# Kernel tuning notes

Measured on AMD Instinct MI355X. Metric: run time of the kernel, lower is better.

The kernel has to match this reference:

```python
import jax, jax.numpy as jnp
import numpy as np
from jax import lax

B, T, I, H, O = 128, 512, 256, 512, 256


def setup_inputs() -> dict:
    key = jax.random.key(0)
    ks = jax.random.split(key, 7)
    s_ih = 1.0 / np.sqrt(H)
    return {
        "inputs": jax.random.normal(ks[0], (B, T, I), dtype=jnp.float32),
        "W_ih": jax.random.uniform(ks[1], (H, I), jnp.float32, -s_ih, s_ih),
        "b_ih": jax.random.uniform(ks[2], (H,), jnp.float32, -s_ih, s_ih),
        "W_hh": jax.random.uniform(ks[3], (H, H), jnp.float32, -s_ih, s_ih),
        "b_hh": jax.random.uniform(ks[4], (H,), jnp.float32, -s_ih, s_ih),
        "W_out": jax.random.uniform(ks[5], (O, H), jnp.float32, -s_ih, s_ih),
        "b_out": jax.random.uniform(ks[6], (O,), jnp.float32, -s_ih, s_ih),
        "h0": jnp.zeros((H,), dtype=jnp.float32),
    }


def reference(inputs, W_ih, b_ih, W_hh, b_hh, W_out, b_out, h0):
    # inputs: [B, T, I]; returns readout of last hidden state: [B, O]
    Bsz, Tlen = inputs.shape[0], inputs.shape[1]
    inv_T = jnp.asarray(1.0 / Tlen, dtype=inputs.dtype)
    # Precompute input projection for all timesteps (one big GEMM):
    # x_proj[b,t,h] = inputs @ W_ih.T + b_ih + b_hh
    x_proj = jnp.einsum('bti,hi->bth', inputs, W_ih) + (b_ih + b_hh)
    x_proj_t = jnp.swapaxes(x_proj, 0, 1)  # [T, B, H]

    def step(h, xp):
        # RNNCell: tanh(xp + h @ W_hh.T); residual scaling by 1/T
        h_new = jnp.tanh(xp + h @ W_hh.T) * inv_T + h
        return h_new, None

    h_init = jnp.broadcast_to(h0, (Bsz, h0.shape[0]))
    h_last, _ = lax.scan(step, h_init, x_proj_t)
    return h_last @ W_out.T + b_out
```

## Files before the change

kernel.cpp:

```cpp
#include <hip/hip_runtime.h>
#include <stdint.h>

#define NB 128
#define NT 512
#define NI 256
#define NH 512
#define NO 256

__device__ __forceinline__ uint16_t f2bf(float x) {
  uint32_t u = __float_as_uint(x);
  return (uint16_t)((u + 0x7fffu + ((u >> 16) & 1u)) >> 16);
}
__device__ __forceinline__ uint32_t pack2bf(float a, float b) {
  return (uint32_t)f2bf(a) | ((uint32_t)f2bf(b) << 16);
}

#if __has_builtin(__builtin_amdgcn_fdot2_f32_bf16)
typedef __bf16 bf16x2_t __attribute__((ext_vector_type(2)));
#define HAVE_DOT2 1
#endif

__device__ __forceinline__ float dot2bf(uint32_t w, uint32_t h, float acc) {
#ifdef HAVE_DOT2
  return __builtin_amdgcn_fdot2_f32_bf16(__builtin_bit_cast(bf16x2_t, w),
                                         __builtin_bit_cast(bf16x2_t, h), acc, false);
#else
  float wl = __uint_as_float(w << 16), wh = __uint_as_float(w & 0xffff0000u);
  float hl = __uint_as_float(h << 16), hh = __uint_as_float(h & 0xffff0000u);
  return fmaf(wh, hh, fmaf(wl, hl, acc));
#endif
}

__device__ __forceinline__ float dot4x(uint4 w, uint4 h, float a) {
  a = dot2bf(w.x, h.x, a);
  a = dot2bf(w.y, h.y, a);
  a = dot2bf(w.z, h.z, a);
  a = dot2bf(w.w, h.w, a);
  return a;
}

__device__ __forceinline__ float fast_tanh(float x) {
  float e = __expf(2.0f * x);
#if __has_builtin(__builtin_amdgcn_rcpf)
  return 1.0f - 2.0f * __builtin_amdgcn_rcpf(e + 1.0f);
#else
  return 1.0f - 2.0f / (e + 1.0f);
#endif
}

typedef __bf16 bf16x8 __attribute__((ext_vector_type(8)));
typedef float f32x4 __attribute__((ext_vector_type(4)));

__global__ __launch_bounds__(256) void prep_kernel(const float* __restrict__ Whh,
                                                   const float* __restrict__ Wih,
                                                   const float* __restrict__ Wout,
                                                   const float* __restrict__ bih,
                                                   const float* __restrict__ bhh,
                                                   uint4* __restrict__ WQ,
                                                   float* __restrict__ WoT,
                                                   uint2* __restrict__ Wihb32,
                                                   float* __restrict__ BS) {
  int idx = blockIdx.x * 256 + threadIdx.x;
  if (idx < 32768) {
    int q = idx >> 9, t = idx & 511;
    int jj = q >> 3, c = q & 7;
    int j = (t & 63) * 8 + jj;
    int k2b = (t >> 6) * 32 + c * 4;
    const float* row = Whh + (size_t)j * NH + 2 * k2b;
    float4 f0 = *(const float4*)row;
    float4 f1 = *(const float4*)(row + 4);
    uint4 w;
    w.x = pack2bf(f0.x, f0.y);
    w.y = pack2bf(f0.z, f0.w);
    w.z = pack2bf(f1.x, f1.y);
    w.w = pack2bf(f1.z, f1.w);
    WQ[idx] = w;
  } else if (idx < 65536) {
    int i = idx - 32768;
    float4 f = *(const float4*)(Wih + (size_t)i * 4);
    uint2 p;
    p.x = pack2bf(f.x, f.y);
    p.y = pack2bf(f.z, f.w);
    Wihb32[i] = p;
  } else if (idx < 98304) {
    int i = idx - 65536;
    int o4 = (i & 63) * 4;
    int k = i >> 6;
    float4 v;
    v.x = Wout[(size_t)(o4 + 0) * NH + k];
    v.y = Wout[(size_t)(o4 + 1) * NH + k];
    v.z = Wout[(size_t)(o4 + 2) * NH + k];
    v.w = Wout[(size_t)(o4 + 3) * NH + k];
    *(float4*)&WoT[(size_t)k * NO + o4] = v;
  } else if (idx < 98816) {
    int n = idx - 98304;
    BS[n] = bih[n] + bhh[n];
  }
}

__global__ __launch_bounds__(256, 2) void xproj_kernel(const float* __restrict__ A,
                                                       const uint16_t* __restrict__ Wihb,
                                                       const float* __restrict__ BS,
                                                       uint16_t* __restrict__ XP) {
  const int w = threadIdx.x >> 6;
  const int l = threadIdx.x & 63;
  const int sl = l & 15, quad = l >> 4;
  const int m = blockIdx.x * 64 + w * 16 + sl;

  f32x4 acc[32] = {};
  const float* arow = A + (size_t)m * NI;

  for (int k0 = 0; k0 < NI; k0 += 32) {
    float4 f0 = *(const float4*)(arow + k0 + quad * 8);
    float4 f1 = *(const float4*)(arow + k0 + quad * 8 + 4);
    uint4 ap;
    ap.x = pack2bf(f0.x, f0.y);
    ap.y = pack2bf(f0.z, f0.w);
    ap.z = pack2bf(f1.x, f1.y);
    ap.w = pack2bf(f1.z, f1.w);
    bf16x8 afrag = __builtin_bit_cast(bf16x8, ap);
#pragma unroll
    for (int u = 0; u < 32; ++u) {
      uint4 bp = *(const uint4*)(Wihb + (size_t)(u * 16 + sl) * NI + k0 + quad * 8);
      acc[u] = __builtin_amdgcn_mfma_f32_16x16x32_bf16(
          __builtin_bit_cast(bf16x8, bp), afrag, acc[u], 0, 0, 0);
    }
  }

  uint16_t* xrow = XP + (size_t)m * NH;
#pragma unroll
  for (int u = 0; u < 32; ++u) {
    float4 bs = *(const float4*)(BS + u * 16 + quad * 4);
    uint2 pw;
    pw.x = pack2bf(acc[u][0] + bs.x, acc[u][1] + bs.y);
    pw.y = pack2bf(acc[u][2] + bs.z, acc[u][3] + bs.w);
    *(uint2*)(xrow + u * 16 + quad * 4) = pw;
  }
}

__global__ __launch_bounds__(512, 2) void recur_kernel(const uint4* __restrict__ WQ,
                                                       const float* __restrict__ WoT,
                                                       const uint16_t* __restrict__ XP,
                                                       const float* __restrict__ h0,
                                                       const float* __restrict__ bout,
                                                       float* __restrict__ out) {
  __shared__ uint4 WL[12][512];
  __shared__ __align__(16) uint16_t h2[2][NH];
  __shared__ float P[8][NH];
  __shared__ float hsf[NH];
  const int t = threadIdx.x;
  const int b = blockIdx.x;
  const int kq8 = t >> 6;
  const int jb = (t & 63) * 8;
  const float invT = 1.0f / (float)NT;

  uint4 Wr[52];
#pragma unroll
  for (int q = 0; q < 52; ++q) Wr[q] = WQ[q * 512 + t];
#pragma unroll
  for (int i = 0; i < 12; ++i) WL[i][t] = WQ[(52 + i) * 512 + t];

  float hj = h0[t];
  h2[0][t] = f2bf(hj);
  __syncthreads();

  const uint16_t* xpb = XP + (size_t)b * NT * NH;

  for (int ts = 0; ts < NT; ++ts) {
    const int cur = ts & 1;
    float xpj = __uint_as_float((uint32_t)xpb[(size_t)ts * NH + t] << 16);

    const uint32_t* hw = (const uint32_t*)h2[cur] + kq8 * 32;
    float a0 = 0.f, a1 = 0.f, a2 = 0.f, a3 = 0.f;
    float a4 = 0.f, a5 = 0.f, a6 = 0.f, a7 = 0.f;

    uint4 hv0 = *(const uint4*)(hw);
    uint4 hv1 = *(const uint4*)(hw + 4);
    uint4 w6n = Wr[48];
    uint4 w7n = WL[4][t];
#pragma unroll
    for (int c = 0; c < 8; ++c) {
      uint4 hv = hv0;
      hv0 = hv1;
      if (c < 6) hv1 = *(const uint4*)(hw + (c + 2) * 4);
      uint4 w6 = w6n, w7 = w7n;
      if (c < 7) {
        w6n = (c + 1 < 4) ? Wr[48 + c + 1] : WL[c - 3][t];
        w7n = WL[5 + c][t];
      }
      a0 = dot4x(Wr[c], hv, a0);
      a1 = dot4x(Wr[8 + c], hv, a1);
      a2 = dot4x(Wr[16 + c], hv, a2);
      a3 = dot4x(Wr[24 + c], hv, a3);
      a4 = dot4x(Wr[32 + c], hv, a4);
      a5 = dot4x(Wr[40 + c], hv, a5);
      a6 = dot4x(w6, hv, a6);
      a7 = dot4x(w7, hv, a7);
    }
    *(float4*)&P[kq8][jb] = make_float4(a0, a1, a2, a3);
    *(float4*)&P[kq8][jb + 4] = make_float4(a4, a5, a6, a7);
    __syncthreads();

    float y = ((P[0][t] + P[1][t]) + (P[2][t] + P[3][t])) +
              ((P[4][t] + P[5][t]) + (P[6][t] + P[7][t]));
    float hnew = fmaf(fast_tanh(xpj + y), invT, hj);
    hj = hnew;
    h2[cur ^ 1][t] = f2bf(hnew);
    __syncthreads();
  }

  hsf[t] = hj;
  __syncthreads();

  if (t < NO) {
    float c0 = 0.f, c1 = 0.f;
#pragma unroll 4
    for (int k = 0; k < NH; k += 2) {
      c0 = fmaf(WoT[(size_t)k * NO + t], hsf[k], c0);
      c1 = fmaf(WoT[(size_t)(k + 1) * NO + t], hsf[k + 1], c1);
    }
    out[(size_t)b * NO + t] = c0 + c1 + bout[t];
  }
}

extern "C" void kernel_launch(void* const* d_in, const int* in_sizes, int n_in,
                              void* d_out, int out_size, void* d_ws, size_t ws_size,
                              hipStream_t stream) {
  const float* inputs = (const float*)d_in[0];
  const float* Wih    = (const float*)d_in[1];
  const float* bih    = (const float*)d_in[2];
  const float* Whh    = (const float*)d_in[3];
  const float* bhh    = (const float*)d_in[4];
  const float* Wout   = (const float*)d_in[5];
  const float* bout   = (const float*)d_in[6];
  const float* h0     = (const float*)d_in[7];
  float* out = (float*)d_out;

  char* ws = (char*)d_ws;
  uint4*    WQ     = (uint4*)ws;
  float*    WoT    = (float*)(ws + (512u << 10));
  uint2*    Wihb32 = (uint2*)(ws + (1024u << 10));
  float*    BS     = (float*)(ws + (1280u << 10));
  uint16_t* XP     = (uint16_t*)(ws + (1536u << 10));

  hipLaunchKernelGGL(prep_kernel, dim3(386), dim3(256), 0, stream,
                     Whh, Wih, Wout, bih, bhh, WQ, WoT, Wihb32, BS);
  hipLaunchKernelGGL(xproj_kernel, dim3(NB * NT / 64), dim3(256), 0, stream,
                     inputs, (const uint16_t*)Wihb32, BS, XP);
  hipLaunchKernelGGL(recur_kernel, dim3(NB), dim3(512), 0, stream,
                     WQ, WoT, XP, h0, bout, out);
}
```

Baseline: 998.9 us.

## Process two batch rows per recurrence block to reuse register-resident W_hh

Each recurrence workgroup now advances two batch sequences at once and launches half as many blocks. Every weight fragment loaded from registers or LDS feeds two dot products, one per sequence. The aim is to halve per-step weight traffic and synchronisation per batch row, and the recurrence is latency-bound, so each block now does roughly twice the work per step. The cost is higher register pressure, since the 52 uint4 weight registers and now 16 accumulators share a launch bound of 2 blocks per CU, plus 64 blocks that may leave CUs idle.

```diff
diff --git a/kernel.cpp b/kernel.cpp
--- a/kernel.cpp
+++ b/kernel.cpp
@@ -145,11 +145,10 @@
                                                        const float* __restrict__ bout,
                                                        float* __restrict__ out) {
   __shared__ uint4 WL[12][512];
-  __shared__ __align__(16) uint16_t h2[2][NH];
-  __shared__ float P[8][NH];
-  __shared__ float hsf[NH];
+  __shared__ __align__(16) uint16_t h2[2][2][NH];
+  __shared__ float P[2][8][NH];
   const int t = threadIdx.x;
-  const int b = blockIdx.x;
+  const int b0 = blockIdx.x * 2;
   const int kq8 = t >> 6;
   const int jb = (t & 63) * 8;
   const float invT = 1.0f / (float)NT;
@@ -160,66 +159,79 @@
 #pragma unroll
   for (int i = 0; i < 12; ++i) WL[i][t] = WQ[(52 + i) * 512 + t];
 
-  float hj = h0[t];
-  h2[0][t] = f2bf(hj);
+  float hjA = h0[t];
+  float hjB = hjA;
+  {
+    uint16_t hb = f2bf(hjA);
+    h2[0][0][t] = hb;
+    h2[0][1][t] = hb;
+  }
   __syncthreads();
 
-  const uint16_t* xpb = XP + (size_t)b * NT * NH;
+  const uint16_t* xpA = XP + (size_t)b0 * NT * NH;
+  const uint16_t* xpB = XP + (size_t)(b0 + 1) * NT * NH;
 
   for (int ts = 0; ts < NT; ++ts) {
     const int cur = ts & 1;
-    float xpj = __uint_as_float((uint32_t)xpb[(size_t)ts * NH + t] << 16);
-
-    const uint32_t* hw = (const uint32_t*)h2[cur] + kq8 * 32;
-    float a0 = 0.f, a1 = 0.f, a2 = 0.f, a3 = 0.f;
-    float a4 = 0.f, a5 = 0.f, a6 = 0.f, a7 = 0.f;
-
-    uint4 hv0 = *(const uint4*)(hw);
-    uint4 hv1 = *(const uint4*)(hw + 4);
-    uint4 w6n = Wr[48];
-    uint4 w7n = WL[4][t];
+    float xA = __uint_as_float((uint32_t)xpA[(size_t)ts * NH + t] << 16);
+    float xB = __uint_as_float((uint32_t)xpB[(size_t)ts * NH + t] << 16);
+
+    const uint32_t* hwA = (const uint32_t*)h2[cur][0] + kq8 * 32;
+    const uint32_t* hwB = (const uint32_t*)h2[cur][1] + kq8 * 32;
+    float aA[8] = {}, aB[8] = {};
 #pragma unroll
     for (int c = 0; c < 8; ++c) {
-      uint4 hv = hv0;
-      hv0 = hv1;
-      if (c < 6) hv1 = *(const uint4*)(hw + (c + 2) * 4);
-      uint4 w6 = w6n, w7 = w7n;
-      if (c < 7) {
-        w6n = (c + 1 < 4) ? Wr[48 + c + 1] : WL[c - 3][t];
-        w7n = WL[5 + c][t];
+      uint4 hA = *(const uint4*)(hwA + c * 4);
+      uint4 hB = *(const uint4*)(hwB + c * 4);
+#pragma unroll
+      for (int jj = 0; jj < 6; ++jj) {
+        uint4 w = Wr[jj * 8 + c];
+        aA[jj] = dot4x(w, hA, aA[jj]);
+        aB[jj] = dot4x(w, hB, aB[jj]);
       }
-      a0 = dot4x(Wr[c], hv, a0);
-      a1 = dot4x(Wr[8 + c], hv, a1);
-      a2 = dot4x(Wr[16 + c], hv, a2);
-      a3 = dot4x(Wr[24 + c], hv, a3);
-      a4 = dot4x(Wr[32 + c], hv, a4);
-      a5 = dot4x(Wr[40 + c], hv, a5);
-      a6 = dot4x(w6, hv, a6);
-      a7 = dot4x(w7, hv, a7);
+      {
+        uint4 w = (c < 4) ? Wr[48 + c] : WL[c - 4][t];
+        aA[6] = dot4x(w, hA, aA[6]);
+        aB[6] = dot4x(w, hB, aB[6]);
+      }
+      {
+        uint4 w = WL[4 + c][t];
+        aA[7] = dot4x(w, hA, aA[7]);
+        aB[7] = dot4x(w, hB, aB[7]);
+      }
     }
-    *(float4*)&P[kq8][jb] = make_float4(a0, a1, a2, a3);
-    *(float4*)&P[kq8][jb + 4] = make_float4(a4, a5, a6, a7);
+    *(float4*)&P[0][kq8][jb]     = make_float4(aA[0], aA[1], aA[2], aA[3]);
+    *(float4*)&P[0][kq8][jb + 4] = make_float4(aA[4], aA[5], aA[6], aA[7]);
+    *(float4*)&P[1][kq8][jb]     = make_float4(aB[0], aB[1], aB[2], aB[3]);
+    *(float4*)&P[1][kq8][jb + 4] = make_float4(aB[4], aB[5], aB[6], aB[7]);
     __syncthreads();
 
-    float y = ((P[0][t] + P[1][t]) + (P[2][t] + P[3][t])) +
-              ((P[4][t] + P[5][t]) + (P[6][t] + P[7][t]));
-    float hnew = fmaf(fast_tanh(xpj + y), invT, hj);
-    hj = hnew;
-    h2[cur ^ 1][t] = f2bf(hnew);
+    float yA = ((P[0][0][t] + P[0][1][t]) + (P[0][2][t] + P[0][3][t])) +
+               ((P[0][4][t] + P[0][5][t]) + (P[0][6][t] + P[0][7][t]));
+    float yB = ((P[1][0][t] + P[1][1][t]) + (P[1][2][t] + P[1][3][t])) +
+               ((P[1][4][t] + P[1][5][t]) + (P[1][6][t] + P[1][7][t]));
+    hjA = fmaf(fast_tanh(xA + yA), invT, hjA);
+    hjB = fmaf(fast_tanh(xB + yB), invT, hjB);
+    h2[cur ^ 1][0][t] = f2bf(hjA);
+    h2[cur ^ 1][1][t] = f2bf(hjB);
     __syncthreads();
   }
 
-  hsf[t] = hj;
+  P[0][0][t] = hjA;
+  P[1][0][t] = hjB;
   __syncthreads();
 
-  if (t < NO) {
+  {
+    const int bb = t >> 8;
+    const int o = t & 255;
+    const float* hs = &P[bb][0][0];
     float c0 = 0.f, c1 = 0.f;
 #pragma unroll 4
     for (int k = 0; k < NH; k += 2) {
-      c0 = fmaf(WoT[(size_t)k * NO + t], hsf[k], c0);
-      c1 = fmaf(WoT[(size_t)(k + 1) * NO + t], hsf[k + 1], c1);
+      c0 = fmaf(WoT[(size_t)k * NO + o], hs[k], c0);
+      c1 = fmaf(WoT[(size_t)(k + 1) * NO + o], hs[k + 1], c1);
     }
-    out[(size_t)b * NO + t] = c0 + c1 + bout[t];
+    out[(size_t)(b0 + bb) * NO + o] = c0 + c1 + bout[o];
   }
 }
 
@@ -247,6 +259,6 @@
                      Whh, Wih, Wout, bih, bhh, WQ, WoT, Wihb32, BS);
   hipLaunchKernelGGL(xproj_kernel, dim3(NB * NT / 64), dim3(256), 0, stream,
                      inputs, (const uint16_t*)Wihb32, BS, XP);
-  hipLaunchKernelGGL(recur_kernel, dim3(NB), dim3(512), 0, stream,
+  hipLaunchKernelGGL(recur_kernel, dim3(NB / 2), dim3(512), 0, stream,
                      WQ, WoT, XP, h0, bout, out);
 }
```

New measurement: 1.672 ms. 1.67x slower.

## Use MFMA for recurrent matvec and pre-swizzle W_ih into fragment layout

Applied to the files above, without the earlier changes.

The per-step h @ W_hh product moves from bf16 dot2 instructions to 16x16x32 bf16 MFMAs. The h vector is broadcast across all rows of the A operand and only element 0 of each accumulator is used. This removes the shared-memory partial-sum array and one barrier per timestep, at the cost of MFMA work that is mostly redundant. W_ih is also repacked into MFMA fragment order, so each lane of the input projection does a single coalesced 16-byte load.

```diff
diff --git a/kernel.cpp b/kernel.cpp
--- a/kernel.cpp
+++ b/kernel.cpp
@@ -13,30 +13,6 @@
 }
 __device__ __forceinline__ uint32_t pack2bf(float a, float b) {
   return (uint32_t)f2bf(a) | ((uint32_t)f2bf(b) << 16);
-}
-
-#if __has_builtin(__builtin_amdgcn_fdot2_f32_bf16)
-typedef __bf16 bf16x2_t __attribute__((ext_vector_type(2)));
-#define HAVE_DOT2 1
-#endif
-
-__device__ __forceinline__ float dot2bf(uint32_t w, uint32_t h, float acc) {
-#ifdef HAVE_DOT2
-  return __builtin_amdgcn_fdot2_f32_bf16(__builtin_bit_cast(bf16x2_t, w),
-                                         __builtin_bit_cast(bf16x2_t, h), acc, false);
-#else
-  float wl = __uint_as_float(w << 16), wh = __uint_as_float(w & 0xffff0000u);
-  float hl = __uint_as_float(h << 16), hh = __uint_as_float(h & 0xffff0000u);
-  return fmaf(wh, hh, fmaf(wl, hl, acc));
-#endif
-}
-
-__device__ __forceinline__ float dot4x(uint4 w, uint4 h, float a) {
-  a = dot2bf(w.x, h.x, a);
-  a = dot2bf(w.y, h.y, a);
-  a = dot2bf(w.z, h.z, a);
-  a = dot2bf(w.w, h.w, a);
-  return a;
 }
 
 __device__ __forceinline__ float fast_tanh(float x) {
@@ -51,39 +27,52 @@
 typedef __bf16 bf16x8 __attribute__((ext_vector_type(8)));
 typedef float f32x4 __attribute__((ext_vector_type(4)));
 
+__device__ __forceinline__ f32x4 mfma16(bf16x8 a, uint4 b, f32x4 c) {
+  return __builtin_amdgcn_mfma_f32_16x16x32_bf16(a, __builtin_bit_cast(bf16x8, b), c, 0, 0, 0);
+}
+
 __global__ __launch_bounds__(256) void prep_kernel(const float* __restrict__ Whh,
                                                    const float* __restrict__ Wih,
                                                    const float* __restrict__ Wout,
                                                    const float* __restrict__ bih,
                                                    const float* __restrict__ bhh,
-                                                   uint4* __restrict__ WQ,
+                                                   uint4* __restrict__ WB,
                                                    float* __restrict__ WoT,
-                                                   uint2* __restrict__ Wihb32,
+                                                   uint4* __restrict__ WihF,
                                                    float* __restrict__ BS) {
   int idx = blockIdx.x * 256 + threadIdx.x;
   if (idx < 32768) {
     int q = idx >> 9, t = idx & 511;
-    int jj = q >> 3, c = q & 7;
-    int j = (t & 63) * 8 + jj;
-    int k2b = (t >> 6) * 32 + c * 4;
-    const float* row = Whh + (size_t)j * NH + 2 * k2b;
+    int u = q >> 4, tk = q & 15;
+    int n = (t >> 6) * 64 + u * 16 + (t & 15);
+    int kb = tk * 32 + ((t >> 4) & 3) * 8;
+    const float* row = Whh + (size_t)n * NH + kb;
     float4 f0 = *(const float4*)row;
     float4 f1 = *(const float4*)(row + 4);
-    uint4 w;
-    w.x = pack2bf(f0.x, f0.y);
-    w.y = pack2bf(f0.z, f0.w);
-    w.z = pack2bf(f1.x, f1.y);
-    w.w = pack2bf(f1.z, f1.w);
-    WQ[idx] = w;
-  } else if (idx < 65536) {
+    uint4 wq;
+    wq.x = pack2bf(f0.x, f0.y);
+    wq.y = pack2bf(f0.z, f0.w);
+    wq.z = pack2bf(f1.x, f1.y);
+    wq.w = pack2bf(f1.z, f1.w);
+    WB[idx] = wq;
+  } else if (idx < 49152) {
     int i = idx - 32768;
-    float4 f = *(const float4*)(Wih + (size_t)i * 4);
-    uint2 p;
-    p.x = pack2bf(f.x, f.y);
-    p.y = pack2bf(f.z, f.w);
-    Wihb32[i] = p;
-  } else if (idx < 98304) {
-    int i = idx - 65536;
+    int l = i & 63;
+    int uk = i >> 6;
+    int k0 = uk & 7, u = uk >> 3;
+    int n = u * 16 + (l & 15);
+    int kb = k0 * 32 + (l >> 4) * 8;
+    const float* row = Wih + (size_t)n * NI + kb;
+    float4 f0 = *(const float4*)row;
+    float4 f1 = *(const float4*)(row + 4);
+    uint4 wq;
+    wq.x = pack2bf(f0.x, f0.y);
+    wq.y = pack2bf(f0.z, f0.w);
+    wq.z = pack2bf(f1.x, f1.y);
+    wq.w = pack2bf(f1.z, f1.w);
+    WihF[i] = wq;
+  } else if (idx < 81920) {
+    int i = idx - 49152;
     int o4 = (i & 63) * 4;
     int k = i >> 6;
     float4 v;
@@ -92,14 +81,14 @@
     v.z = Wout[(size_t)(o4 + 2) * NH + k];
     v.w = Wout[(size_t)(o4 + 3) * NH + k];
     *(float4*)&WoT[(size_t)k * NO + o4] = v;
-  } else if (idx < 98816) {
-    int n = idx - 98304;
+  } else if (idx < 82432) {
+    int n = idx - 81920;
     BS[n] = bih[n] + bhh[n];
   }
 }
 
 __global__ __launch_bounds__(256, 2) void xproj_kernel(const float* __restrict__ A,
-                                                       const uint16_t* __restrict__ Wihb,
+                                                       const uint4* __restrict__ WihF,
                                                        const float* __restrict__ BS,
                                                        uint16_t* __restrict__ XP) {
   const int w = threadIdx.x >> 6;
@@ -110,9 +99,9 @@
   f32x4 acc[32] = {};
   const float* arow = A + (size_t)m * NI;
 
-  for (int k0 = 0; k0 < NI; k0 += 32) {
-    float4 f0 = *(const float4*)(arow + k0 + quad * 8);
-    float4 f1 = *(const float4*)(arow + k0 + quad * 8 + 4);
+  for (int k0 = 0; k0 < 8; ++k0) {
+    float4 f0 = *(const float4*)(arow + k0 * 32 + quad * 8);
+    float4 f1 = *(const float4*)(arow + k0 * 32 + quad * 8 + 4);
     uint4 ap;
     ap.x = pack2bf(f0.x, f0.y);
     ap.y = pack2bf(f0.z, f0.w);
@@ -121,7 +110,7 @@
     bf16x8 afrag = __builtin_bit_cast(bf16x8, ap);
 #pragma unroll
     for (int u = 0; u < 32; ++u) {
-      uint4 bp = *(const uint4*)(Wihb + (size_t)(u * 16 + sl) * NI + k0 + quad * 8);
+      uint4 bp = WihF[(u * 8 + k0) * 64 + l];
       acc[u] = __builtin_amdgcn_mfma_f32_16x16x32_bf16(
           __builtin_bit_cast(bf16x8, bp), afrag, acc[u], 0, 0, 0);
     }
@@ -138,7 +127,7 @@
   }
 }
 
-__global__ __launch_bounds__(512, 2) void recur_kernel(const uint4* __restrict__ WQ,
+__global__ __launch_bounds__(512, 2) void recur_kernel(const uint4* __restrict__ WB,
                                                        const float* __restrict__ WoT,
                                                        const uint16_t* __restrict__ XP,
                                                        const float* __restrict__ h0,
@@ -146,70 +135,49 @@
                                                        float* __restrict__ out) {
   __shared__ uint4 WL[12][512];
   __shared__ __align__(16) uint16_t h2[2][NH];
-  __shared__ float P[8][NH];
   __shared__ float hsf[NH];
   const int t = threadIdx.x;
   const int b = blockIdx.x;
-  const int kq8 = t >> 6;
-  const int jb = (t & 63) * 8;
+  const int w = t >> 6;
+  const int sl = t & 15, quad = (t >> 4) & 3;
+  const int myn = w * 64 + quad * 16 + sl;
   const float invT = 1.0f / (float)NT;
 
   uint4 Wr[52];
 #pragma unroll
-  for (int q = 0; q < 52; ++q) Wr[q] = WQ[q * 512 + t];
-#pragma unroll
-  for (int i = 0; i < 12; ++i) WL[i][t] = WQ[(52 + i) * 512 + t];
-
-  float hj = h0[t];
-  h2[0][t] = f2bf(hj);
+  for (int q = 0; q < 52; ++q) Wr[q] = WB[q * 512 + t];
+#pragma unroll
+  for (int i = 0; i < 12; ++i) WL[i][t] = WB[(52 + i) * 512 + t];
+
+  float hj = h0[myn];
+  h2[0][myn] = f2bf(hj);
   __syncthreads();
 
-  const uint16_t* xpb = XP + (size_t)b * NT * NH;
+  const uint16_t* xpb = XP + (size_t)b * NT * NH + myn;
 
   for (int ts = 0; ts < NT; ++ts) {
     const int cur = ts & 1;
-    float xpj = __uint_as_float((uint32_t)xpb[(size_t)ts * NH + t] << 16);
-
-    const uint32_t* hw = (const uint32_t*)h2[cur] + kq8 * 32;
-    float a0 = 0.f, a1 = 0.f, a2 = 0.f, a3 = 0.f;
-    float a4 = 0.f, a5 = 0.f, a6 = 0.f, a7 = 0.f;
-
-    uint4 hv0 = *(const uint4*)(hw);
-    uint4 hv1 = *(const uint4*)(hw + 4);
-    uint4 w6n = Wr[48];
-    uint4 w7n = WL[4][t];
-#pragma unroll
-    for (int c = 0; c < 8; ++c) {
-      uint4 hv = hv0;
-      hv0 = hv1;
-      if (c < 6) hv1 = *(const uint4*)(hw + (c + 2) * 4);
-      uint4 w6 = w6n, w7 = w7n;
-      if (c < 7) {
-        w6n = (c + 1 < 4) ? Wr[48 + c + 1] : WL[c - 3][t];
-        w7n = WL[5 + c][t];
-      }
-      a0 = dot4x(Wr[c], hv, a0);
-      a1 = dot4x(Wr[8 + c], hv, a1);
-      a2 = dot4x(Wr[16 + c], hv, a2);
-      a3 = dot4x(Wr[24 + c], hv, a3);
-      a4 = dot4x(Wr[32 + c], hv, a4);
-      a5 = dot4x(Wr[40 + c], hv, a5);
-      a6 = dot4x(w6, hv, a6);
-      a7 = dot4x(w7, hv, a7);
+    float xpj = __uint_as_float((uint32_t)xpb[(size_t)ts * NH] << 16);
+
+    const uint16_t* hbuf = h2[cur];
+    f32x4 acc0 = {}, acc1 = {}, acc2 = {}, acc3 = {};
+#pragma unroll
+    for (int tk = 0; tk < 16; ++tk) {
+      bf16x8 hfrag = *(const bf16x8*)(hbuf + tk * 32 + quad * 8);
+      acc0 = mfma16(hfrag, Wr[tk], acc0);
+      acc1 = mfma16(hfrag, Wr[16 + tk], acc1);
+      acc2 = mfma16(hfrag, Wr[32 + tk], acc2);
+      uint4 w3 = (tk < 4) ? Wr[48 + tk] : WL[tk - 4][t];
+      acc3 = mfma16(hfrag, w3, acc3);
     }
-    *(float4*)&P[kq8][jb] = make_float4(a0, a1, a2, a3);
-    *(float4*)&P[kq8][jb + 4] = make_float4(a4, a5, a6, a7);
-    __syncthreads();
-
-    float y = ((P[0][t] + P[1][t]) + (P[2][t] + P[3][t])) +
-              ((P[4][t] + P[5][t]) + (P[6][t] + P[7][t]));
+    float y = (quad == 0) ? acc0[0] : (quad == 1) ? acc1[0] : (quad == 2) ? acc2[0] : acc3[0];
     float hnew = fmaf(fast_tanh(xpj + y), invT, hj);
     hj = hnew;
-    h2[cur ^ 1][t] = f2bf(hnew);
+    h2[cur ^ 1][myn] = f2bf(hnew);
     __syncthreads();
   }
 
-  hsf[t] = hj;
+  hsf[myn] = hj;
   __syncthreads();
 
   if (t < NO) {
@@ -237,16 +205,16 @@
   float* out = (float*)d_out;
 
   char* ws = (char*)d_ws;
-  uint4*    WQ     = (uint4*)ws;
-  float*    WoT    = (float*)(ws + (512u << 10));
-  uint2*    Wihb32 = (uint2*)(ws + (1024u << 10));
-  float*    BS     = (float*)(ws + (1280u << 10));
-  uint16_t* XP     = (uint16_t*)(ws + (1536u << 10));
-
-  hipLaunchKernelGGL(prep_kernel, dim3(386), dim3(256), 0, stream,
-                     Whh, Wih, Wout, bih, bhh, WQ, WoT, Wihb32, BS);
+  uint4*    WB   = (uint4*)ws;
+  float*    WoT  = (float*)(ws + (512u << 10));
+  uint4*    WihF = (uint4*)(ws + (1024u << 10));
+  float*    BS   = (float*)(ws + (1280u << 10));
+  uint16_t* XP   = (uint16_t*)(ws + (1536u << 10));
+
+  hipLaunchKernelGGL(prep_kernel, dim3(322), dim3(256), 0, stream,
+                     Whh, Wih, Wout, bih, bhh, WB, WoT, WihF, BS);
   hipLaunchKernelGGL(xproj_kernel, dim3(NB * NT / 64), dim3(256), 0, stream,
-                     inputs, (const uint16_t*)Wihb32, BS, XP);
+                     inputs, WihF, BS, XP);
   hipLaunchKernelGGL(recur_kernel, dim3(NB), dim3(512), 0, stream,
-                     WQ, WoT, XP, h0, bout, out);
-}
+                     WB, WoT, XP, h0, bout, out);
+}
```

After: 943.2 us. 5.6% less time.
